# Performance work log

Hardware: AMD Instinct MI355X
Metric: run time of the kernel (lower is better)

## Reference

```python
import jax, jax.numpy as jnp
import numpy as np

N, C, E = 50000, 64, 800000
EPS = 1e-5

def _ln(h, g, b):
    mu = jnp.mean(h, axis=-1, keepdims=True)
    var = jnp.var(h, axis=-1, keepdims=True)
    return (h - mu) * jax.lax.rsqrt(var + EPS) * g + b

def setup_inputs() -> dict:
    key = jax.random.key(0)
    ks = jax.random.split(key, 16)
    def w(k, i, o):
        return jax.random.normal(k, (i, o), jnp.float32) * (1.0 / np.sqrt(i))
    return {
        "x": jax.random.normal(ks[0], (N, C), jnp.float32),
        "edge_index": jax.random.randint(ks[1], (2, E), 0, N, jnp.int32),
        # structure_predictor: Linear(2C,256) -> LN(256) -> GELU -> Dropout(eval) -> Linear(256,1)
        "sp_w1": w(ks[2], 2 * C, 256), "sp_b1": jnp.zeros((256,), jnp.float32),
        "sp_g": jnp.ones((256,), jnp.float32), "sp_be": jnp.zeros((256,), jnp.float32),
        "sp_w2": w(ks[3], 256, 1), "sp_b2": jnp.zeros((1,), jnp.float32),
        # feature_reconstructor: Linear(C,2C) -> LN(2C) -> GELU -> Dropout(eval) -> Linear(2C,C)
        "fr_w1": w(ks[4], C, 2 * C), "fr_b1": jnp.zeros((2 * C,), jnp.float32),
        "fr_g": jnp.ones((2 * C,), jnp.float32), "fr_be": jnp.zeros((2 * C,), jnp.float32),
        "fr_w2": w(ks[5], 2 * C, C), "fr_b2": jnp.zeros((C,), jnp.float32),
        # projection_head: Linear(C,256) -> LN(256) -> GELU -> Linear(256,128)
        "ph_w1": w(ks[6], C, 256), "ph_b1": jnp.zeros((256,), jnp.float32),
        "ph_g": jnp.ones((256,), jnp.float32), "ph_be": jnp.zeros((256,), jnp.float32),
        "ph_w2": w(ks[7], 256, 128), "ph_b2": jnp.zeros((128,), jnp.float32),
    }

def reference(x, edge_index, sp_w1, sp_b1, sp_g, sp_be, sp_w2, sp_b2,
              fr_w1, fr_b1, fr_g, fr_be, fr_w2, fr_b2,
              ph_w1, ph_b1, ph_g, ph_be, ph_w2, ph_b2):
    row, col = edge_index[0], edge_index[1]
    edge_features = jnp.concatenate([x[row], x[col]], axis=1)  # [E, 2C]
    h = _ln(edge_features @ sp_w1 + sp_b1, sp_g, sp_be)
    structure_pred = jax.nn.gelu(h, approximate=False) @ sp_w2 + sp_b2  # [E, 1]
    h = _ln(x @ fr_w1 + fr_b1, fr_g, fr_be)
    reconstructed = jax.nn.gelu(h, approximate=False) @ fr_w2 + fr_b2  # [N, C]
    h = _ln(x @ ph_w1 + ph_b1, ph_g, ph_be)
    projected = jax.nn.gelu(h, approximate=False) @ ph_w2 + ph_b2  # [N, 128]
    return (structure_pred, reconstructed, projected)
```

## Files before the change

kernel.cpp:

```cpp
#include <hip/hip_runtime.h>
#include <hip/hip_bf16.h>

typedef __attribute__((ext_vector_type(8))) short short8;
typedef __attribute__((ext_vector_type(4))) float f32x4;

#define MFMA(a, b, c) __builtin_amdgcn_mfma_f32_16x16x32_bf16((a), (b), (c), 0, 0, 0)

__device__ __forceinline__ unsigned short f2bf(float f) {
    unsigned int u = __float_as_uint(f);
    u += 0x7fffu + ((u >> 16) & 1u);
    return (unsigned short)(u >> 16);
}

template<int CTRL>
__device__ __forceinline__ float dpp_addf(float v) {
    int t = __builtin_amdgcn_update_dpp(0, __float_as_int(v), CTRL, 0xF, 0xF, true);
    return v + __int_as_float(t);
}
__device__ __forceinline__ float rowsum16(float v) {
    v = dpp_addf<0x121>(v);
    v = dpp_addf<0x122>(v);
    v = dpp_addf<0x124>(v);
    v = dpp_addf<0x128>(v);
    return v;
}

__device__ __forceinline__ float gelu_fast(float x) {
    x = __builtin_amdgcn_fmed3f(x, -8.0f, 8.0f);
    float a = x * __builtin_fmaf(x * x, 0.07135533f, 1.59576912f);
    float E = __expf(a);
    float r = __builtin_amdgcn_rcpf(E + 1.0f);
    return x * E * r;
}

__device__ __forceinline__ short8 load_bfrag(const float* __restrict__ w, int k0, int n, int ldn) {
    short8 r;
#pragma unroll
    for (int u = 0; u < 8; ++u)
        r[u] = (short)f2bf(w[(k0 + u) * ldn + n]);
    return r;
}

template<int N1P>
struct SmemMlp {
    unsigned short sS[64 * N1P];
    float rstat[64 * 8];
};

template<int K, int N1, int N2>
__device__ void mlp_role(SmemMlp<N1 + 8>& sm, const float* __restrict__ x,
                         const float* __restrict__ w1, const float* __restrict__ b1,
                         const float* __restrict__ g, const float* __restrict__ be,
                         const float* __restrict__ w2, const float* __restrict__ b2,
                         float* __restrict__ out, int Nrows, int bid, int nblocks) {
    constexpr int KP = K + 8, N1P = N1 + 8;
    constexpr int CPW1 = N1 / 4;
    constexpr int JT1 = CPW1 / 16;
    constexpr int KK1 = K / 32;
    constexpr int KK2 = N1 / 32;
    constexpr int JT2 = N2 / 64;

    const int tid = threadIdx.x;
    const int wave = tid >> 6, lane = tid & 63;
    const int l15 = lane & 15, quad = lane >> 4;

    short8 breg1[JT1][KK1];
#pragma unroll
    for (int j = 0; j < JT1; ++j)
#pragma unroll
        for (int kk = 0; kk < KK1; ++kk)
            breg1[j][kk] = load_bfrag(w1, kk * 32 + quad * 8, CPW1 * wave + 16 * j + l15, N1);

    float b1v[JT1], gv[JT1], bev[JT1];
#pragma unroll
    for (int j = 0; j < JT1; ++j) {
        int c = CPW1 * wave + 16 * j + l15;
        b1v[j] = b1[c]; gv[j] = g[c]; bev[j] = be[c];
    }
    float b2v[JT2];
#pragma unroll
    for (int j = 0; j < JT2; ++j) b2v[j] = b2[wave * 16 * JT2 + 16 * j + l15];

    const int ntiles = (Nrows + 63) >> 6;
    const int m0 = tid >> 2, pp = tid & 3;

    for (int t = bid; t < ntiles; t += nblocks) {
        const int r0 = t << 6;
        __syncthreads();
        {
            int rowg = r0 + m0; if (rowg >= Nrows) rowg = Nrows - 1;
            const float4* src = (const float4*)(x + (long)rowg * K + pp * 16);
            unsigned short* dst = &sm.sS[m0 * KP + pp * 16];
#pragma unroll
            for (int u = 0; u < 4; ++u) {
                float4 f = src[u];
                ushort4 h; h.x = f2bf(f.x); h.y = f2bf(f.y); h.z = f2bf(f.z); h.w = f2bf(f.w);
                *(ushort4*)(dst + 4 * u) = h;
            }
        }
        __syncthreads();

        f32x4 acc1[4][JT1];
#pragma unroll
        for (int i = 0; i < 4; ++i)
#pragma unroll
            for (int j = 0; j < JT1; ++j)
                acc1[i][j] = (f32x4){0.f, 0.f, 0.f, 0.f};

#pragma unroll
        for (int kk = 0; kk < KK1; ++kk) {
            short8 a[4];
#pragma unroll
            for (int i = 0; i < 4; ++i)
                a[i] = *(const short8*)&sm.sS[(16 * i + l15) * KP + kk * 32 + quad * 8];
#pragma unroll
            for (int i = 0; i < 4; ++i)
#pragma unroll
                for (int j = 0; j < JT1; ++j)
                    acc1[i][j] = MFMA(a[i], breg1[j][kk], acc1[i][j]);
        }

#pragma unroll
        for (int i = 0; i < 4; ++i)
#pragma unroll
            for (int r = 0; r < 4; ++r) {
                float s = 0.f, ss = 0.f;
#pragma unroll
                for (int j = 0; j < JT1; ++j) {
                    float v = acc1[i][j][r] + b1v[j];
                    acc1[i][j][r] = v;
                    s += v; ss = __builtin_fmaf(v, v, ss);
                }
                s = rowsum16(s); ss = rowsum16(ss);
                if (l15 == 0) {
                    int row = 16 * i + quad * 4 + r;
                    *(float2*)&sm.rstat[row * 8 + wave * 2] = make_float2(s, ss);
                }
            }
        __syncthreads();

#pragma unroll
        for (int i = 0; i < 4; ++i)
#pragma unroll
            for (int r = 0; r < 4; ++r) {
                int row = 16 * i + quad * 4 + r;
                const float4* st = (const float4*)&sm.rstat[row * 8];
                float4 q0 = st[0], q1 = st[1];
                float s  = (q0.x + q0.z) + (q1.x + q1.z);
                float ss = (q0.y + q0.w) + (q1.y + q1.w);
                float mean = s * (1.f / (float)N1);
                float var  = __builtin_fmaf(ss, 1.f / (float)N1, -mean * mean);
                float rstd = __builtin_amdgcn_rsqf(var + 1e-5f);
                float nm = -mean * rstd;
#pragma unroll
                for (int j = 0; j < JT1; ++j) {
                    float tt = __builtin_fmaf(acc1[i][j][r], rstd, nm);
                    float xn = __builtin_fmaf(tt, gv[j], bev[j]);
                    sm.sS[row * N1P + CPW1 * wave + 16 * j + l15] = f2bf(gelu_fast(xn));
                }
            }
        __syncthreads();

        short8 breg2[JT2][KK2];
#pragma unroll
        for (int j = 0; j < JT2; ++j)
#pragma unroll
            for (int kk = 0; kk < KK2; ++kk)
                breg2[j][kk] = load_bfrag(w2, kk * 32 + quad * 8, wave * 16 * JT2 + 16 * j + l15, N2);

        f32x4 acc2[4][JT2];
#pragma unroll
        for (int i = 0; i < 4; ++i)
#pragma unroll
            for (int j = 0; j < JT2; ++j)
                acc2[i][j] = (f32x4){0.f, 0.f, 0.f, 0.f};

#pragma unroll
        for (int kk = 0; kk < KK2; ++kk) {
            short8 a[4];
#pragma unroll
            for (int i = 0; i < 4; ++i)
                a[i] = *(const short8*)&sm.sS[(16 * i + l15) * N1P + kk * 32 + quad * 8];
#pragma unroll
            for (int i = 0; i < 4; ++i)
#pragma unroll
                for (int j = 0; j < JT2; ++j)
                    acc2[i][j] = MFMA(a[i], breg2[j][kk], acc2[i][j]);
        }

#pragma unroll
        for (int i = 0; i < 4; ++i)
#pragma unroll
            for (int r = 0; r < 4; ++r) {
                int rowg = r0 + 16 * i + quad * 4 + r;
                if (rowg < Nrows) {
#pragma unroll
                    for (int j = 0; j < JT2; ++j)
                        out[(long)rowg * N2 + wave * 16 * JT2 + 16 * j + l15] = acc2[i][j][r] + b2v[j];
                }
            }
    }
}

__device__ void proj_role(unsigned short* sX , const float* __restrict__ x,
                          const float* __restrict__ w1, const float* __restrict__ b1,
                          unsigned short* __restrict__ P, int N, int tile, int isB) {
    constexpr int KP = 72;
    const int tid = threadIdx.x;
    const int wave = tid >> 6, lane = tid & 63;
    const int l15 = lane & 15, quad = lane >> 4;

    short8 breg[4][2];
#pragma unroll
    for (int j = 0; j < 4; ++j)
#pragma unroll
        for (int kk = 0; kk < 2; ++kk)
            breg[j][kk] = load_bfrag(w1, isB * 64 + kk * 32 + quad * 8, wave * 64 + 16 * j + l15, 256);

    float b1v[4];
#pragma unroll
    for (int j = 0; j < 4; ++j)
        b1v[j] = isB ? 0.f : b1[wave * 64 + 16 * j + l15];

    const int r0 = tile * 64;
    {
        int m0 = tid >> 2, pp = tid & 3;
        int rowg = r0 + m0; if (rowg >= N) rowg = N - 1;
        const float4* src = (const float4*)(x + (long)rowg * 64 + pp * 16);
        unsigned short* dst = &sX[m0 * KP + pp * 16];
#pragma unroll
        for (int u = 0; u < 4; ++u) {
            float4 f = src[u];
            ushort4 h; h.x = f2bf(f.x); h.y = f2bf(f.y); h.z = f2bf(f.z); h.w = f2bf(f.w);
            *(ushort4*)(dst + 4 * u) = h;
        }
    }
    __syncthreads();

    f32x4 acc[4][4];
#pragma unroll
    for (int i = 0; i < 4; ++i)
#pragma unroll
        for (int j = 0; j < 4; ++j)
            acc[i][j] = (f32x4){0.f, 0.f, 0.f, 0.f};

#pragma unroll
    for (int kk = 0; kk < 2; ++kk) {
        short8 a[4];
#pragma unroll
        for (int i = 0; i < 4; ++i)
            a[i] = *(const short8*)&sX[(16 * i + l15) * KP + kk * 32 + quad * 8];
#pragma unroll
        for (int i = 0; i < 4; ++i)
#pragma unroll
            for (int j = 0; j < 4; ++j)
                acc[i][j] = MFMA(a[i], breg[j][kk], acc[i][j]);
    }

#pragma unroll
    for (int i = 0; i < 4; ++i)
#pragma unroll
        for (int r = 0; r < 4; ++r) {
            int rowg = r0 + 16 * i + quad * 4 + r;
            if (rowg < N) {
#pragma unroll
                for (int j = 0; j < 4; ++j)
                    P[(long)rowg * 256 + wave * 64 + 16 * j + l15] = f2bf(acc[i][j][r] + b1v[j]);
            }
        }
}

union SmemPrep {
    SmemMlp<136> a;
    SmemMlp<264> b;
    unsigned short sX[64 * 72];
};

__global__ __launch_bounds__(256)
void prep_kernel(const float* __restrict__ x,
                 const float* __restrict__ sp_w1, const float* __restrict__ sp_b1,
                 const float* __restrict__ fr_w1, const float* __restrict__ fr_b1,
                 const float* __restrict__ fr_g, const float* __restrict__ fr_be,
                 const float* __restrict__ fr_w2, const float* __restrict__ fr_b2,
                 const float* __restrict__ ph_w1, const float* __restrict__ ph_b1,
                 const float* __restrict__ ph_g, const float* __restrict__ ph_be,
                 const float* __restrict__ ph_w2, const float* __restrict__ ph_b2,
                 unsigned short* __restrict__ Pa, unsigned short* __restrict__ Pb,
                 float* __restrict__ out_rec, float* __restrict__ out_proj,
                 int N, int ntN) {
    __shared__ SmemPrep sm;
    const int b = blockIdx.x;
    if (b < 128) {
        mlp_role<64, 128, 64>(sm.a, x, fr_w1, fr_b1, fr_g, fr_be, fr_w2, fr_b2,
                              out_rec, N, b, 128);
    } else if (b < 256) {
        mlp_role<64, 256, 128>(sm.b, x, ph_w1, ph_b1, ph_g, ph_be, ph_w2, ph_b2,
                               out_proj, N, b - 128, 128);
    } else {
        int pb = b - 256;
        int isB = pb >= ntN;
        int tile = isB ? pb - ntN : pb;
        proj_role(sm.sX, x, sp_w1, sp_b1, isB ? Pb : Pa, N, tile, isB);
    }
}

__global__ __launch_bounds__(256)
void edge_stream(const unsigned short* __restrict__ Pa, const unsigned short* __restrict__ Pb,
                 const int* __restrict__ ei,
                 const float* __restrict__ g, const float* __restrict__ be,
                 const float* __restrict__ w2, const float* __restrict__ b2,
                 float* __restrict__ out, int E) {
    const int tid = threadIdx.x;
    const int lane = tid & 63;
    const int quad = lane >> 4, l15 = lane & 15;

    float gv[16], bev[16], w2v[16];
    {
        const float4* gp = (const float4*)(g + l15 * 16);
        const float4* bp = (const float4*)(be + l15 * 16);
        const float4* wp = (const float4*)(w2 + l15 * 16);
#pragma unroll
        for (int u = 0; u < 4; ++u) {
            float4 gq = gp[u], bq = bp[u], wq = wp[u];
            gv[4*u+0] = gq.x; gv[4*u+1] = gq.y; gv[4*u+2] = gq.z; gv[4*u+3] = gq.w;
            bev[4*u+0] = bq.x; bev[4*u+1] = bq.y; bev[4*u+2] = bq.z; bev[4*u+3] = bq.w;
            w2v[4*u+0] = wq.x; w2v[4*u+1] = wq.y; w2v[4*u+2] = wq.z; w2v[4*u+3] = wq.w;
        }
    }
    const float b2v = b2[0];

    const int wid = blockIdx.x * 4 + (tid >> 6);
    const int nw = gridDim.x * 4;

    for (long base = (long)wid * 4; base < E; base += (long)nw * 4) {
        long eL = base + quad;
        bool ok = eL < E;
        int e = ok ? (int)eL : E - 1;
        int ir = ei[e], ic = ei[E + e];

        const uint4* pa = (const uint4*)(Pa + (long)ir * 256 + l15 * 16);
        const uint4* pb = (const uint4*)(Pb + (long)ic * 256 + l15 * 16);
        uint4 A0 = pa[0], A1 = pa[1];
        uint4 B0 = pb[0], B1 = pb[1];

        unsigned int av[8] = {A0.x, A0.y, A0.z, A0.w, A1.x, A1.y, A1.z, A1.w};
        unsigned int bv[8] = {B0.x, B0.y, B0.z, B0.w, B1.x, B1.y, B1.z, B1.w};

        float h[16];
#pragma unroll
        for (int k = 0; k < 8; ++k) {
            float alo = __uint_as_float(av[k] << 16);
            float ahi = __uint_as_float(av[k] & 0xffff0000u);
            float blo = __uint_as_float(bv[k] << 16);
            float bhi = __uint_as_float(bv[k] & 0xffff0000u);
            h[2*k]   = alo + blo;
            h[2*k+1] = ahi + bhi;
        }

        float s = 0.f, ss = 0.f;
#pragma unroll
        for (int u = 0; u < 16; ++u) {
            s += h[u];
            ss = __builtin_fmaf(h[u], h[u], ss);
        }
        s = rowsum16(s); ss = rowsum16(ss);

        float mean = s * (1.f / 256.f);
        float var  = __builtin_fmaf(ss, 1.f / 256.f, -mean * mean);
        float rstd = __builtin_amdgcn_rsqf(var + 1e-5f);
        float nm = -mean * rstd;

        float spp = 0.f;
#pragma unroll
        for (int u = 0; u < 16; ++u) {
            float tt = __builtin_fmaf(h[u], rstd, nm);
            float xn = __builtin_fmaf(tt, gv[u], bev[u]);
            spp = __builtin_fmaf(gelu_fast(xn), w2v[u], spp);
        }
        spp = rowsum16(spp);
        if (l15 == 0 && ok) out[eL] = spp + b2v;
    }
}

struct SmemEdge {
    unsigned short sA[2][32 * 136];
    float rstat[32 * 8];
    float spL[32 * 4];
};
union SmemU {
    SmemEdge e;
    SmemMlp<136> a;
    SmemMlp<264> b;
};

__device__ void edge_role(SmemEdge& sm, const float* __restrict__ x, const int* __restrict__ ei,
                          const float* __restrict__ w1, const float* __restrict__ b1,
                          const float* __restrict__ g, const float* __restrict__ be,
                          const float* __restrict__ w2, const float* __restrict__ b2,
                          float* __restrict__ out, int E, int bid, int nblocks) {
    constexpr int KP = 136;
    const int tid = threadIdx.x;
    const int cw = tid >> 6, lane = tid & 63;
    const int l15 = lane & 15, quad = lane >> 4;

    short8 breg[4][4];
#pragma unroll
    for (int j = 0; j < 4; ++j)
#pragma unroll
        for (int kk = 0; kk < 4; ++kk)
            breg[j][kk] = load_bfrag(w1, kk * 32 + quad * 8, cw * 64 + 16 * j + l15, 256);

    float b1v[4], gv[4], bev[4], w2v[4];
#pragma unroll
    for (int j = 0; j < 4; ++j) {
        int c = cw * 64 + 16 * j + l15;
        b1v[j] = b1[c]; gv[j] = g[c]; bev[j] = be[c]; w2v[j] = w2[c];
    }
    const float b2v = b2[0];

    const int ntiles = (E + 31) >> 5;
    const int eLoc = tid >> 3, p = tid & 7;
    const int node = p >> 2, foff = (p & 3) * 16;

    float4 pf[4];
    auto issue = [&](int t) {
        int e = t * 32 + eLoc; if (e >= E) e = E - 1;
        int idx = ei[node * E + e];
        const float4* src = (const float4*)(x + (long)idx * 64 + foff);
#pragma unroll
        for (int u = 0; u < 4; ++u) pf[u] = src[u];
    };
    auto stage = [&](int buf) {
        unsigned short* dst = &sm.sA[buf][eLoc * KP + node * 64 + foff];
#pragma unroll
        for (int u = 0; u < 4; ++u) {
            ushort4 h;
            h.x = f2bf(pf[u].x); h.y = f2bf(pf[u].y);
            h.z = f2bf(pf[u].z); h.w = f2bf(pf[u].w);
            *(ushort4*)(dst + 4 * u) = h;
        }
    };

    int t = bid;
    if (t >= ntiles) return;
    issue(t); stage(0);
    if (t + nblocks < ntiles) issue(t + nblocks);
    __syncthreads();
    int cur = 0;

    for (; t < ntiles; t += nblocks) {
        f32x4 acc[2][4];
#pragma unroll
        for (int i = 0; i < 2; ++i)
#pragma unroll
            for (int j = 0; j < 4; ++j)
                acc[i][j] = (f32x4){0.f, 0.f, 0.f, 0.f};

#pragma unroll
        for (int kk = 0; kk < 4; ++kk) {
            short8 a[2];
#pragma unroll
            for (int i = 0; i < 2; ++i)
                a[i] = *(const short8*)&sm.sA[cur][(16 * i + l15) * KP + kk * 32 + quad * 8];
#pragma unroll
            for (int i = 0; i < 2; ++i)
#pragma unroll
                for (int j = 0; j < 4; ++j)
                    acc[i][j] = MFMA(a[i], breg[j][kk], acc[i][j]);
        }

        if (t + nblocks < ntiles) {
            stage(cur ^ 1);
            if (t + 2 * nblocks < ntiles) issue(t + 2 * nblocks);
        }

#pragma unroll
        for (int i = 0; i < 2; ++i)
#pragma unroll
            for (int r = 0; r < 4; ++r) {
                float v0 = acc[i][0][r] + b1v[0];
                float v1 = acc[i][1][r] + b1v[1];
                float v2 = acc[i][2][r] + b1v[2];
                float v3 = acc[i][3][r] + b1v[3];
                acc[i][0][r] = v0; acc[i][1][r] = v1; acc[i][2][r] = v2; acc[i][3][r] = v3;
                float s  = (v0 + v1) + (v2 + v3);
                float ss = __builtin_fmaf(v0, v0, __builtin_fmaf(v1, v1,
                           __builtin_fmaf(v2, v2, v3 * v3)));
                s = rowsum16(s); ss = rowsum16(ss);
                if (l15 == 0) {
                    int row = 16 * i + quad * 4 + r;
                    *(float2*)&sm.rstat[row * 8 + cw * 2] = make_float2(s, ss);
                }
            }
        __syncthreads();

#pragma unroll
        for (int i = 0; i < 2; ++i)
#pragma unroll
            for (int r = 0; r < 4; ++r) {
                int row = 16 * i + quad * 4 + r;
                const float4* st = (const float4*)&sm.rstat[row * 8];
                float4 q0 = st[0], q1 = st[1];
                float s  = (q0.x + q0.z) + (q1.x + q1.z);
                float ss = (q0.y + q0.w) + (q1.y + q1.w);
                float mean = s * (1.f / 256.f);
                float var  = __builtin_fmaf(ss, 1.f / 256.f, -mean * mean);
                float rstd = __builtin_amdgcn_rsqf(var + 1e-5f);
                float nm = -mean * rstd;
                float spp = 0.f;
#pragma unroll
                for (int j = 0; j < 4; ++j) {
                    float tt = __builtin_fmaf(acc[i][j][r], rstd, nm);
                    float xn = __builtin_fmaf(tt, gv[j], bev[j]);
                    spp = __builtin_fmaf(gelu_fast(xn), w2v[j], spp);
                }
                spp = rowsum16(spp);
                if (l15 == 0) sm.spL[row * 4 + cw] = spp;
            }
        __syncthreads();

        if (tid < 32) {
            int e = t * 32 + tid;
            if (e < E) {
                const float4* sp = (const float4*)&sm.spL[tid * 4];
                float4 u0 = sp[0];
                out[e] = ((u0.x + u0.y) + (u0.z + u0.w)) + b2v;
            }
        }
        cur ^= 1;
    }
}

__global__ __launch_bounds__(256, 3)
void fused_all(const float* __restrict__ x, const int* __restrict__ ei,
               const float* __restrict__ sp_w1, const float* __restrict__ sp_b1,
               const float* __restrict__ sp_g, const float* __restrict__ sp_be,
               const float* __restrict__ sp_w2, const float* __restrict__ sp_b2,
               const float* __restrict__ fr_w1, const float* __restrict__ fr_b1,
               const float* __restrict__ fr_g, const float* __restrict__ fr_be,
               const float* __restrict__ fr_w2, const float* __restrict__ fr_b2,
               const float* __restrict__ ph_w1, const float* __restrict__ ph_b1,
               const float* __restrict__ ph_g, const float* __restrict__ ph_be,
               const float* __restrict__ ph_w2, const float* __restrict__ ph_b2,
               float* __restrict__ out_sp, float* __restrict__ out_rec,
               float* __restrict__ out_proj, int N, int E) {
    __shared__ SmemU sm;
    const int b = blockIdx.x;
    if (b < 128) {
        mlp_role<64, 128, 64>(sm.a, x, fr_w1, fr_b1, fr_g, fr_be, fr_w2, fr_b2,
                              out_rec, N, b, 128);
    } else if (b < 256) {
        mlp_role<64, 256, 128>(sm.b, x, ph_w1, ph_b1, ph_g, ph_be, ph_w2, ph_b2,
                               out_proj, N, b - 128, 128);
    } else {
        edge_role(sm.e, x, ei, sp_w1, sp_b1, sp_g, sp_be, sp_w2, sp_b2,
                  out_sp, E, b - 256, 1024);
    }
}

extern "C" void kernel_launch(void* const* d_in, const int* in_sizes, int n_in,
                              void* d_out, int out_size, void* d_ws, size_t ws_size,
                              hipStream_t stream) {
    const float* x     = (const float*)d_in[0];
    const int*   ei    = (const int*)d_in[1];
    const float* sp_w1 = (const float*)d_in[2];
    const float* sp_b1 = (const float*)d_in[3];
    const float* sp_g  = (const float*)d_in[4];
    const float* sp_be = (const float*)d_in[5];
    const float* sp_w2 = (const float*)d_in[6];
    const float* sp_b2 = (const float*)d_in[7];
    const float* fr_w1 = (const float*)d_in[8];
    const float* fr_b1 = (const float*)d_in[9];
    const float* fr_g  = (const float*)d_in[10];
    const float* fr_be = (const float*)d_in[11];
    const float* fr_w2 = (const float*)d_in[12];
    const float* fr_b2 = (const float*)d_in[13];
    const float* ph_w1 = (const float*)d_in[14];
    const float* ph_b1 = (const float*)d_in[15];
    const float* ph_g  = (const float*)d_in[16];
    const float* ph_be = (const float*)d_in[17];
    const float* ph_w2 = (const float*)d_in[18];
    const float* ph_b2 = (const float*)d_in[19];

    const int N = in_sizes[0] / 64;
    const int E = in_sizes[1] / 2;

    float* out_sp   = (float*)d_out;
    float* out_rec  = out_sp + E;
    float* out_proj = out_rec + (size_t)N * 64;

    const size_t needed = 2ull * (size_t)N * 256 * sizeof(unsigned short);
    if (ws_size >= needed) {
        unsigned short* Pa = (unsigned short*)d_ws;
        unsigned short* Pb = Pa + (size_t)N * 256;
        const int ntN = (N + 63) / 64;

        prep_kernel<<<dim3(256 + 2 * ntN), dim3(256), 0, stream>>>(
            x, sp_w1, sp_b1,
            fr_w1, fr_b1, fr_g, fr_be, fr_w2, fr_b2,
            ph_w1, ph_b1, ph_g, ph_be, ph_w2, ph_b2,
            Pa, Pb, out_rec, out_proj, N, ntN);

        edge_stream<<<dim3(2048), dim3(256), 0, stream>>>(
            Pa, Pb, ei, sp_g, sp_be, sp_w2, sp_b2, out_sp, E);
    } else {
        fused_all<<<dim3(1280), dim3(256), 0, stream>>>(
            x, ei, sp_w1, sp_b1, sp_g, sp_be, sp_w2, sp_b2,
            fr_w1, fr_b1, fr_g, fr_be, fr_w2, fr_b2,
            ph_w1, ph_b1, ph_g, ph_be, ph_w2, ph_b2,
            out_sp, out_rec, out_proj, N, E);
    }
}
```

Before: 306.0 us.

## Split projection into own kernel and overlap node MLPs with pipelined edge stream

Moves the per-node edge projections (Pa/Pb) into a separate small kernel that computes both halves per tile from one staged x tile. The node MLPs (reconstructor, projection head) then share a single launch with the edge streaming blocks, so the edge work overlaps the MLP work instead of running after it. The edge loop now software-pipelines its index and row gathers two iterations ahead to hide gather latency. GELU is rewritten with exp2 and a single fma, which removes a few ALU ops per element. The costs are higher register pressure from the prefetched rows and some load imbalance between the two kinds of blocks in the fused launch.

```diff
diff --git a/kernel.cpp b/kernel.cpp
--- a/kernel.cpp
+++ b/kernel.cpp
@@ -25,12 +25,18 @@
     return v;
 }
 
+#if __has_builtin(__builtin_amdgcn_exp2f)
+#define EXP2(x) __builtin_amdgcn_exp2f(x)
+#else
+#define EXP2(x) __expf((x) * 0.69314718f)
+#endif
+
 __device__ __forceinline__ float gelu_fast(float x) {
     x = __builtin_amdgcn_fmed3f(x, -8.0f, 8.0f);
-    float a = x * __builtin_fmaf(x * x, 0.07135533f, 1.59576912f);
-    float E = __expf(a);
+    float a = x * __builtin_fmaf(x * x, 0.10295427f, 2.3021210f);
+    float E = EXP2(a);
     float r = __builtin_amdgcn_rcpf(E + 1.0f);
-    return x * E * r;
+    return __builtin_fmaf(-x, r, x);
 }
 
 __device__ __forceinline__ short8 load_bfrag(const float* __restrict__ w, int k0, int n, int ldn) {
@@ -202,27 +208,17 @@
     }
 }
 
-__device__ void proj_role(unsigned short* sX , const float* __restrict__ x,
-                          const float* __restrict__ w1, const float* __restrict__ b1,
-                          unsigned short* __restrict__ P, int N, int tile, int isB) {
+__global__ __launch_bounds__(256)
+void proj_kernel(const float* __restrict__ x, const float* __restrict__ w1,
+                 const float* __restrict__ b1, unsigned short* __restrict__ Pa,
+                 unsigned short* __restrict__ Pb, int N) {
     constexpr int KP = 72;
+    __shared__ unsigned short sX[64 * KP];
     const int tid = threadIdx.x;
     const int wave = tid >> 6, lane = tid & 63;
     const int l15 = lane & 15, quad = lane >> 4;
-
-    short8 breg[4][2];
-#pragma unroll
-    for (int j = 0; j < 4; ++j)
-#pragma unroll
-        for (int kk = 0; kk < 2; ++kk)
-            breg[j][kk] = load_bfrag(w1, isB * 64 + kk * 32 + quad * 8, wave * 64 + 16 * j + l15, 256);
-
-    float b1v[4];
-#pragma unroll
-    for (int j = 0; j < 4; ++j)
-        b1v[j] = isB ? 0.f : b1[wave * 64 + 16 * j + l15];
-
-    const int r0 = tile * 64;
+    const int r0 = blockIdx.x * 64;
+
     {
         int m0 = tid >> 2, pp = tid & 3;
         int rowg = r0 + m0; if (rowg >= N) rowg = N - 1;
@@ -237,57 +233,171 @@
     }
     __syncthreads();
 
-    f32x4 acc[4][4];
-#pragma unroll
-    for (int i = 0; i < 4; ++i)
+    for (int isB = 0; isB < 2; ++isB) {
+        unsigned short* __restrict__ P = isB ? Pb : Pa;
+
+        short8 breg[4][2];
 #pragma unroll
         for (int j = 0; j < 4; ++j)
-            acc[i][j] = (f32x4){0.f, 0.f, 0.f, 0.f};
-
-#pragma unroll
-    for (int kk = 0; kk < 2; ++kk) {
-        short8 a[4];
+#pragma unroll
+            for (int kk = 0; kk < 2; ++kk)
+                breg[j][kk] = load_bfrag(w1, isB * 64 + kk * 32 + quad * 8, wave * 64 + 16 * j + l15, 256);
+
+        float b1v[4];
+#pragma unroll
+        for (int j = 0; j < 4; ++j)
+            b1v[j] = isB ? 0.f : b1[wave * 64 + 16 * j + l15];
+
+        f32x4 acc[4][4];
 #pragma unroll
         for (int i = 0; i < 4; ++i)
-            a[i] = *(const short8*)&sX[(16 * i + l15) * KP + kk * 32 + quad * 8];
+#pragma unroll
+            for (int j = 0; j < 4; ++j)
+                acc[i][j] = (f32x4){0.f, 0.f, 0.f, 0.f};
+
+#pragma unroll
+        for (int kk = 0; kk < 2; ++kk) {
+            short8 a[4];
+#pragma unroll
+            for (int i = 0; i < 4; ++i)
+                a[i] = *(const short8*)&sX[(16 * i + l15) * KP + kk * 32 + quad * 8];
+#pragma unroll
+            for (int i = 0; i < 4; ++i)
+#pragma unroll
+                for (int j = 0; j < 4; ++j)
+                    acc[i][j] = MFMA(a[i], breg[j][kk], acc[i][j]);
+        }
+
 #pragma unroll
         for (int i = 0; i < 4; ++i)
 #pragma unroll
-            for (int j = 0; j < 4; ++j)
-                acc[i][j] = MFMA(a[i], breg[j][kk], acc[i][j]);
-    }
-
-#pragma unroll
-    for (int i = 0; i < 4; ++i)
-#pragma unroll
-        for (int r = 0; r < 4; ++r) {
-            int rowg = r0 + 16 * i + quad * 4 + r;
-            if (rowg < N) {
-#pragma unroll
-                for (int j = 0; j < 4; ++j)
-                    P[(long)rowg * 256 + wave * 64 + 16 * j + l15] = f2bf(acc[i][j][r] + b1v[j]);
-            }
-        }
+            for (int r = 0; r < 4; ++r) {
+                int rowg = r0 + 16 * i + quad * 4 + r;
+                if (rowg < N) {
+#pragma unroll
+                    for (int j = 0; j < 4; ++j)
+                        P[(long)rowg * 256 + wave * 64 + 16 * j + l15] = f2bf(acc[i][j][r] + b1v[j]);
+                }
+            }
+    }
+}
+
+__device__ __forceinline__ int clamp_e(long v, int E) {
+    return v < (long)E ? (int)v : E - 1;
+}
+
+__device__ void edge_role2(const unsigned short* __restrict__ Pa,
+                           const unsigned short* __restrict__ Pb,
+                           const int* __restrict__ ei,
+                           const float* __restrict__ g, const float* __restrict__ be,
+                           const float* __restrict__ w2, const float* __restrict__ b2,
+                           float* __restrict__ out, int E, int ebid, int nebk) {
+    const int tid = threadIdx.x;
+    const int lane = tid & 63;
+    const int quad = lane >> 4, l15 = lane & 15;
+
+    float gv[16], bev[16], w2v[16];
+    {
+        const float4* gp = (const float4*)(g + l15 * 16);
+        const float4* bp = (const float4*)(be + l15 * 16);
+        const float4* wp = (const float4*)(w2 + l15 * 16);
+#pragma unroll
+        for (int u = 0; u < 4; ++u) {
+            float4 gq = gp[u], bq = bp[u], wq = wp[u];
+            gv[4*u+0] = gq.x; gv[4*u+1] = gq.y; gv[4*u+2] = gq.z; gv[4*u+3] = gq.w;
+            bev[4*u+0] = bq.x; bev[4*u+1] = bq.y; bev[4*u+2] = bq.z; bev[4*u+3] = bq.w;
+            w2v[4*u+0] = wq.x; w2v[4*u+1] = wq.y; w2v[4*u+2] = wq.z; w2v[4*u+3] = wq.w;
+        }
+    }
+    const float b2v = b2[0];
+
+    const int wid = ebid * 4 + (tid >> 6);
+    const long stride = (long)nebk * 16L;
+    long base = (long)wid * 4;
+    if (base >= E) return;
+
+    int ir1, ic1;
+    uint4 cA0, cA1, cB0, cB1;
+    {
+        int e0 = clamp_e(base + quad, E);
+        int r = ei[e0], c = ei[E + e0];
+        const uint4* pa = (const uint4*)(Pa + (long)r * 256 + l15 * 16);
+        const uint4* pb = (const uint4*)(Pb + (long)c * 256 + l15 * 16);
+        cA0 = pa[0]; cA1 = pa[1]; cB0 = pb[0]; cB1 = pb[1];
+        int e1 = clamp_e(base + stride + quad, E);
+        ir1 = ei[e1]; ic1 = ei[E + e1];
+    }
+
+    for (; base < E; base += stride) {
+        int e2 = clamp_e(base + 2 * stride + quad, E);
+        int ir2 = ei[e2];
+        int ic2 = ei[E + e2];
+        const uint4* pa = (const uint4*)(Pa + (long)ir1 * 256 + l15 * 16);
+        const uint4* pb = (const uint4*)(Pb + (long)ic1 * 256 + l15 * 16);
+        uint4 nA0 = pa[0], nA1 = pa[1], nB0 = pb[0], nB1 = pb[1];
+
+        unsigned int av[8] = {cA0.x, cA0.y, cA0.z, cA0.w, cA1.x, cA1.y, cA1.z, cA1.w};
+        unsigned int bv[8] = {cB0.x, cB0.y, cB0.z, cB0.w, cB1.x, cB1.y, cB1.z, cB1.w};
+
+        float h[16];
+#pragma unroll
+        for (int k = 0; k < 8; ++k) {
+            float alo = __uint_as_float(av[k] << 16);
+            float ahi = __uint_as_float(av[k] & 0xffff0000u);
+            float blo = __uint_as_float(bv[k] << 16);
+            float bhi = __uint_as_float(bv[k] & 0xffff0000u);
+            h[2*k]   = alo + blo;
+            h[2*k+1] = ahi + bhi;
+        }
+
+        float s = 0.f, ss = 0.f;
+#pragma unroll
+        for (int u = 0; u < 16; ++u) {
+            s += h[u];
+            ss = __builtin_fmaf(h[u], h[u], ss);
+        }
+        s = rowsum16(s); ss = rowsum16(ss);
+
+        float mean = s * (1.f / 256.f);
+        float var  = __builtin_fmaf(ss, 1.f / 256.f, -mean * mean);
+        float rstd = __builtin_amdgcn_rsqf(var + 1e-5f);
+        float nm = -mean * rstd;
+
+        float spp = 0.f;
+#pragma unroll
+        for (int u = 0; u < 16; ++u) {
+            float tt = __builtin_fmaf(h[u], rstd, nm);
+            float xn = __builtin_fmaf(tt, gv[u], bev[u]);
+            spp = __builtin_fmaf(gelu_fast(xn), w2v[u], spp);
+        }
+        spp = rowsum16(spp);
+        long eL = base + quad;
+        if (l15 == 0 && eL < E) out[eL] = spp + b2v;
+
+        cA0 = nA0; cA1 = nA1; cB0 = nB0; cB1 = nB1;
+        ir1 = ir2; ic1 = ic2;
+    }
 }
 
 union SmemPrep {
     SmemMlp<136> a;
     SmemMlp<264> b;
-    unsigned short sX[64 * 72];
 };
 
 __global__ __launch_bounds__(256)
-void prep_kernel(const float* __restrict__ x,
-                 const float* __restrict__ sp_w1, const float* __restrict__ sp_b1,
-                 const float* __restrict__ fr_w1, const float* __restrict__ fr_b1,
-                 const float* __restrict__ fr_g, const float* __restrict__ fr_be,
-                 const float* __restrict__ fr_w2, const float* __restrict__ fr_b2,
-                 const float* __restrict__ ph_w1, const float* __restrict__ ph_b1,
-                 const float* __restrict__ ph_g, const float* __restrict__ ph_be,
-                 const float* __restrict__ ph_w2, const float* __restrict__ ph_b2,
-                 unsigned short* __restrict__ Pa, unsigned short* __restrict__ Pb,
-                 float* __restrict__ out_rec, float* __restrict__ out_proj,
-                 int N, int ntN) {
+void fused_main(const float* __restrict__ x,
+                const unsigned short* __restrict__ Pa, const unsigned short* __restrict__ Pb,
+                const int* __restrict__ ei,
+                const float* __restrict__ sp_g, const float* __restrict__ sp_be,
+                const float* __restrict__ sp_w2, const float* __restrict__ sp_b2,
+                const float* __restrict__ fr_w1, const float* __restrict__ fr_b1,
+                const float* __restrict__ fr_g, const float* __restrict__ fr_be,
+                const float* __restrict__ fr_w2, const float* __restrict__ fr_b2,
+                const float* __restrict__ ph_w1, const float* __restrict__ ph_b1,
+                const float* __restrict__ ph_g, const float* __restrict__ ph_be,
+                const float* __restrict__ ph_w2, const float* __restrict__ ph_b2,
+                float* __restrict__ out_sp, float* __restrict__ out_rec,
+                float* __restrict__ out_proj, int N, int E, int nebk) {
     __shared__ SmemPrep sm;
     const int b = blockIdx.x;
     if (b < 128) {
@@ -297,88 +407,7 @@
         mlp_role<64, 256, 128>(sm.b, x, ph_w1, ph_b1, ph_g, ph_be, ph_w2, ph_b2,
                                out_proj, N, b - 128, 128);
     } else {
-        int pb = b - 256;
-        int isB = pb >= ntN;
-        int tile = isB ? pb - ntN : pb;
-        proj_role(sm.sX, x, sp_w1, sp_b1, isB ? Pb : Pa, N, tile, isB);
-    }
-}
-
-__global__ __launch_bounds__(256)
-void edge_stream(const unsigned short* __restrict__ Pa, const unsigned short* __restrict__ Pb,
-                 const int* __restrict__ ei,
-                 const float* __restrict__ g, const float* __restrict__ be,
-                 const float* __restrict__ w2, const float* __restrict__ b2,
-                 float* __restrict__ out, int E) {
-    const int tid = threadIdx.x;
-    const int lane = tid & 63;
-    const int quad = lane >> 4, l15 = lane & 15;
-
-    float gv[16], bev[16], w2v[16];
-    {
-        const float4* gp = (const float4*)(g + l15 * 16);
-        const float4* bp = (const float4*)(be + l15 * 16);
-        const float4* wp = (const float4*)(w2 + l15 * 16);
-#pragma unroll
-        for (int u = 0; u < 4; ++u) {
-            float4 gq = gp[u], bq = bp[u], wq = wp[u];
-            gv[4*u+0] = gq.x; gv[4*u+1] = gq.y; gv[4*u+2] = gq.z; gv[4*u+3] = gq.w;
-            bev[4*u+0] = bq.x; bev[4*u+1] = bq.y; bev[4*u+2] = bq.z; bev[4*u+3] = bq.w;
-            w2v[4*u+0] = wq.x; w2v[4*u+1] = wq.y; w2v[4*u+2] = wq.z; w2v[4*u+3] = wq.w;
-        }
-    }
-    const float b2v = b2[0];
-
-    const int wid = blockIdx.x * 4 + (tid >> 6);
-    const int nw = gridDim.x * 4;
-
-    for (long base = (long)wid * 4; base < E; base += (long)nw * 4) {
-        long eL = base + quad;
-        bool ok = eL < E;
-        int e = ok ? (int)eL : E - 1;
-        int ir = ei[e], ic = ei[E + e];
-
-        const uint4* pa = (const uint4*)(Pa + (long)ir * 256 + l15 * 16);
-        const uint4* pb = (const uint4*)(Pb + (long)ic * 256 + l15 * 16);
-        uint4 A0 = pa[0], A1 = pa[1];
-        uint4 B0 = pb[0], B1 = pb[1];
-
-        unsigned int av[8] = {A0.x, A0.y, A0.z, A0.w, A1.x, A1.y, A1.z, A1.w};
-        unsigned int bv[8] = {B0.x, B0.y, B0.z, B0.w, B1.x, B1.y, B1.z, B1.w};
-
-        float h[16];
-#pragma unroll
-        for (int k = 0; k < 8; ++k) {
-            float alo = __uint_as_float(av[k] << 16);
-            float ahi = __uint_as_float(av[k] & 0xffff0000u);
-            float blo = __uint_as_float(bv[k] << 16);
-            float bhi = __uint_as_float(bv[k] & 0xffff0000u);
-            h[2*k]   = alo + blo;
-            h[2*k+1] = ahi + bhi;
-        }
-
-        float s = 0.f, ss = 0.f;
-#pragma unroll
-        for (int u = 0; u < 16; ++u) {
-            s += h[u];
-            ss = __builtin_fmaf(h[u], h[u], ss);
-        }
-        s = rowsum16(s); ss = rowsum16(ss);
-
-        float mean = s * (1.f / 256.f);
-        float var  = __builtin_fmaf(ss, 1.f / 256.f, -mean * mean);
-        float rstd = __builtin_amdgcn_rsqf(var + 1e-5f);
-        float nm = -mean * rstd;
-
-        float spp = 0.f;
-#pragma unroll
-        for (int u = 0; u < 16; ++u) {
-            float tt = __builtin_fmaf(h[u], rstd, nm);
-            float xn = __builtin_fmaf(tt, gv[u], bev[u]);
-            spp = __builtin_fmaf(gelu_fast(xn), w2v[u], spp);
-        }
-        spp = rowsum16(spp);
-        if (l15 == 0 && ok) out[eL] = spp + b2v;
+        edge_role2(Pa, Pb, ei, sp_g, sp_be, sp_w2, sp_b2, out_sp, E, b - 256, nebk);
     }
 }
 
@@ -594,15 +623,15 @@
         unsigned short* Pa = (unsigned short*)d_ws;
         unsigned short* Pb = Pa + (size_t)N * 256;
         const int ntN = (N + 63) / 64;
-
-        prep_kernel<<<dim3(256 + 2 * ntN), dim3(256), 0, stream>>>(
-            x, sp_w1, sp_b1,
+        const int NEB = 2048;
+
+        proj_kernel<<<dim3(ntN), dim3(256), 0, stream>>>(x, sp_w1, sp_b1, Pa, Pb, N);
+
+        fused_main<<<dim3(256 + NEB), dim3(256), 0, stream>>>(
+            x, Pa, Pb, ei, sp_g, sp_be, sp_w2, sp_b2,
             fr_w1, fr_b1, fr_g, fr_be, fr_w2, fr_b2,
             ph_w1, ph_b1, ph_g, ph_be, ph_w2, ph_b2,
-            Pa, Pb, out_rec, out_proj, N, ntN);
-
-        edge_stream<<<dim3(2048), dim3(256), 0, stream>>>(
-            Pa, Pb, ei, sp_g, sp_be, sp_w2, sp_b2, out_sp, E);
+            out_sp, out_rec, out_proj, N, E, NEB);
     } else {
         fused_all<<<dim3(1280), dim3(256), 0, stream>>>(
             x, ei, sp_w1, sp_b1, sp_g, sp_be, sp_w2, sp_b2,
```

Result: slower. 344.6 us (+12.6%).
